# Optimization experiments

Measured on AMD Instinct MI355X. Metric: run time of the kernel, lower is better.

The kernel has to match this reference:

```python
import jax, jax.numpy as jnp
import numpy as np

N_NODES = 100000
N_EDGES = 1600000
IN_DIM = 128
OUT_DIM = 128
N_HEADS = 4


def setup_inputs() -> dict:
    key = jax.random.key(0)
    k1, k2, k3, k4, k5 = jax.random.split(key, 5)
    h = jax.random.normal(k1, (N_NODES, IN_DIM), dtype=jnp.float32)
    src = jax.random.randint(k2, (N_EDGES,), 0, N_NODES, dtype=jnp.int32)
    dst = jax.random.randint(k3, (N_EDGES,), 0, N_NODES, dtype=jnp.int32)
    s = 1.0 / np.sqrt(IN_DIM)
    W_self = jax.random.normal(k4, (N_HEADS, IN_DIM, OUT_DIM), dtype=jnp.float32) * s
    W_neigh = jax.random.normal(k5, (N_HEADS, IN_DIM, OUT_DIM), dtype=jnp.float32) * s
    b = jnp.zeros((N_HEADS, OUT_DIM), dtype=jnp.float32)
    return {"h": h, "src": src, "dst": dst, "W_self": W_self, "W_neigh": W_neigh, "b": b}


def reference(h, src, dst, W_self, W_neigh, b):
    # Mean neighbor aggregation (shared across heads: SAGEConv 'mean' aggregates
    # raw features, then applies per-head linear layers).
    neigh_sum = jax.ops.segment_sum(h[src], dst, num_segments=N_NODES)   # [N, d_in]
    deg = jax.ops.segment_sum(jnp.ones_like(src, dtype=h.dtype), dst,
                              num_segments=N_NODES)                      # [N]
    h_neigh = neigh_sum / jnp.maximum(deg, 1.0)[:, None]                  # [N, d_in]

    # Per-head: fc_self(h_dst) + fc_neigh(h_neigh) + bias -> [H, N, d_out]
    out = (jnp.einsum('nd,hdo->hno', h, W_self)
           + jnp.einsum('nd,hdo->hno', h_neigh, W_neigh)
           + b[:, None, :])
    # merge='mean': average heads
    return jnp.mean(out, axis=0)  # [N, d_out]
```

## Files before the change

kernel.cpp:

```cpp
#include <hip/hip_runtime.h>

#define N_NODES 100000
#define N_EDGES 1600000
#define DIM 128
#define NH 4

#define NPB 512
#define NB 196
#define CAP 12288
#define BCHUNK 8192
#define BEPT 32
#define NBLK ((N_EDGES + BCHUNK - 1) / BCHUNK)

typedef __attribute__((ext_vector_type(8))) short bf16x8;
typedef __attribute__((ext_vector_type(4))) float f32x4;
typedef __attribute__((ext_vector_type(8))) unsigned short u16x8;

#define B_BCUR   0u
#define B_ROWOFF 4096u
#define B_CSR    405504u
#define B_WPACK  6805504u
#define B_BAVG   6871040u
#define B_HB     6871552u
#define NEED_BF16 32869376ull

__device__ inline unsigned short f2bf(float x) {
    union { float f; unsigned u; } v; v.f = x;
    unsigned r = v.u + 0x7fffu + ((v.u >> 16) & 1u);
    return (unsigned short)(r >> 16);
}

template <bool BF>
__global__ __launch_bounds__(256) void prep_kernel(
    const float* __restrict__ h, unsigned short* __restrict__ hb,
    const float* __restrict__ Ws, const float* __restrict__ Wn,
    const float* __restrict__ b, unsigned short* __restrict__ wpack,
    float* __restrict__ bavg, int* __restrict__ bcur) {
    const int t = threadIdx.x;
    if (blockIdx.x == 0) bcur[t] = t * CAP;
    int i = blockIdx.x * 256 + t;
    if (i < DIM * DIM) {
        float s = 0.f, n = 0.f;
#pragma unroll
        for (int hh = 0; hh < NH; ++hh) {
            s += Ws[hh * DIM * DIM + i];
            n += Wn[hh * DIM * DIM + i];
        }
        s *= 0.25f; n *= 0.25f;
        int k = i >> 7, o = i & 127;
        int nt = o >> 4, lanelo = o & 15;
        int ks = k >> 5, lanehi = (k & 31) >> 3, e = k & 7;
        int pos = (((nt * 4 + ks) * 64) + lanehi * 16 + lanelo) * 8 + e;
        wpack[pos] = f2bf(s);
        wpack[16384 + pos] = f2bf(n);
    }
    if (i < DIM) {
        float bb = 0.f;
#pragma unroll
        for (int hh = 0; hh < NH; ++hh) bb += b[hh * DIM + i];
        bavg[i] = 0.25f * bb;
    }
    if (BF) {
        const float4* p = reinterpret_cast<const float4*>(h) + (size_t)i * 2;
        float4 a = p[0], c = p[1];
        u16x8 r;
        r[0] = f2bf(a.x); r[1] = f2bf(a.y); r[2] = f2bf(a.z); r[3] = f2bf(a.w);
        r[4] = f2bf(c.x); r[5] = f2bf(c.y); r[6] = f2bf(c.z); r[7] = f2bf(c.w);
        reinterpret_cast<u16x8*>(hb)[i] = r;
    }
}

__global__ __launch_bounds__(256) void bucket_scatter_kernel(const int* __restrict__ src,
                                                             const int* __restrict__ dst,
                                                             int* __restrict__ bcur,
                                                             int* __restrict__ ebuf) {
    __shared__ int stage[BCHUNK];
    __shared__ unsigned char bkt[BCHUNK];
    __shared__ int lc[256], lbase[256], lpos[256];
    int t = threadIdx.x;
    lc[t] = 0;
    lpos[t] = 0;
    __syncthreads();
    int e0 = blockIdx.x * BCHUNK;
#pragma unroll 4
    for (int j = 0; j < BEPT; ++j) {
        int e = e0 + j * 256 + t;
        if (e < N_EDGES) {
            int d = dst[e];
            stage[j * 256 + t] = (src[e] << 9) | (d & (NPB - 1));
            bkt[j * 256 + t] = (unsigned char)(d >> 9);
            atomicAdd(&lc[d >> 9], 1);
        }
    }
    __syncthreads();
    if (lc[t]) lbase[t] = atomicAdd(&bcur[t], lc[t]);
    __syncthreads();
#pragma unroll 4
    for (int j = 0; j < BEPT; ++j) {
        int e = e0 + j * 256 + t;
        if (e < N_EDGES) {
            int bb = bkt[j * 256 + t];
            int o = atomicAdd(&lpos[bb], 1);
            ebuf[lbase[bb] + o] = stage[j * 256 + t];
        }
    }
}

__global__ __launch_bounds__(256) void csr_build_kernel(const int* __restrict__ bcur,
                                                        const int* __restrict__ ebuf,
                                                        int* __restrict__ rowoff,
                                                        int* __restrict__ csr) {
    __shared__ int hh[NPB], off[NPB], cur[NPB], ss[256];
    int b = blockIdx.x, t = threadIdx.x;
    int cnt = bcur[b] - b * CAP;
    int ibase = b * CAP;
    ss[t] = bcur[t] - t * CAP;
    __syncthreads();
    for (int o = 1; o < 256; o <<= 1) {
        int add = (t >= o) ? ss[t - o] : 0;
        __syncthreads();
        ss[t] += add;
        __syncthreads();
    }
    int obase = ss[b] - cnt;
    hh[t] = 0; hh[t + 256] = 0;
    cur[t] = 0; cur[t + 256] = 0;
    __syncthreads();
    for (int i = t; i < cnt; i += 256) atomicAdd(&hh[ebuf[ibase + i] & (NPB - 1)], 1);
    __syncthreads();
    int e0 = hh[2 * t], e1 = hh[2 * t + 1];
    ss[t] = e0 + e1;
    __syncthreads();
    for (int o = 1; o < 256; o <<= 1) {
        int add = (t >= o) ? ss[t - o] : 0;
        __syncthreads();
        ss[t] += add;
        __syncthreads();
    }
    int ex = ss[t] - (e0 + e1);
    off[2 * t] = ex;
    off[2 * t + 1] = ex + e0;
    __syncthreads();
    int n0 = b * NPB;
#pragma unroll
    for (int k = 0; k < 2; ++k) {
        int s2 = 2 * t + k;
        int n = n0 + s2;
        int dgv = (k == 0) ? e0 : e1;
        if (n < N_NODES) rowoff[n] = ((obase + off[s2]) << 9) | min(dgv, 511);
    }
    for (int i = t; i < cnt; i += 256) {
        int p = ebuf[ibase + i];
        int nl = p & (NPB - 1);
        int o = atomicAdd(&cur[nl], 1);
        csr[obase + off[nl] + o] = p >> 9;
    }
}

template <bool BF>
__global__ __launch_bounds__(1024, 8) void gather_gemm_kernel(
    const float* __restrict__ h, const unsigned short* __restrict__ hb,
    const int* __restrict__ rowoff, const int* __restrict__ csr,
    float* __restrict__ out, const unsigned short* __restrict__ wpack,
    const float* __restrict__ bavg) {
    __shared__ unsigned short hnl[16][DIM + 8];
    const int lane = threadIdx.x & 63;
    const int w = threadIdx.x >> 6;
    const int nb = blockIdx.x * 16;

    {
        const int node = nb + w;
        const int g = lane >> 4;
        const int c = lane & 15;
        const int pw = rowoff[node];
        const int lo = pw >> 9, dg = pw & 511, hi = lo + dg;
        float a0 = 0.f, a1 = 0.f, a2 = 0.f, a3 = 0.f;
        float a4 = 0.f, a5 = 0.f, a6 = 0.f, a7 = 0.f;
        if (BF) {
            int k = lo + g;
            for (; k + 4 < hi; k += 8) {
                int s0 = csr[k], s1 = csr[k + 4];
                uint4 v = *reinterpret_cast<const uint4*>(hb + (size_t)s0 * DIM + c * 8);
                uint4 u = *reinterpret_cast<const uint4*>(hb + (size_t)s1 * DIM + c * 8);
                a0 += __uint_as_float(v.x << 16) + __uint_as_float(u.x << 16);
                a1 += __uint_as_float(v.x & 0xffff0000u) + __uint_as_float(u.x & 0xffff0000u);
                a2 += __uint_as_float(v.y << 16) + __uint_as_float(u.y << 16);
                a3 += __uint_as_float(v.y & 0xffff0000u) + __uint_as_float(u.y & 0xffff0000u);
                a4 += __uint_as_float(v.z << 16) + __uint_as_float(u.z << 16);
                a5 += __uint_as_float(v.z & 0xffff0000u) + __uint_as_float(u.z & 0xffff0000u);
                a6 += __uint_as_float(v.w << 16) + __uint_as_float(u.w << 16);
                a7 += __uint_as_float(v.w & 0xffff0000u) + __uint_as_float(u.w & 0xffff0000u);
            }
            if (k < hi) {
                uint4 v = *reinterpret_cast<const uint4*>(hb + (size_t)csr[k] * DIM + c * 8);
                a0 += __uint_as_float(v.x << 16);
                a1 += __uint_as_float(v.x & 0xffff0000u);
                a2 += __uint_as_float(v.y << 16);
                a3 += __uint_as_float(v.y & 0xffff0000u);
                a4 += __uint_as_float(v.z << 16);
                a5 += __uint_as_float(v.z & 0xffff0000u);
                a6 += __uint_as_float(v.w << 16);
                a7 += __uint_as_float(v.w & 0xffff0000u);
            }
        } else {
            for (int k = lo + g; k < hi; k += 4) {
                const float4* p = reinterpret_cast<const float4*>(h + (size_t)csr[k] * DIM + c * 8);
                float4 x = p[0], y = p[1];
                a0 += x.x; a1 += x.y; a2 += x.z; a3 += x.w;
                a4 += y.x; a5 += y.y; a6 += y.z; a7 += y.w;
            }
        }
        a0 += __shfl_xor(a0, 16, 64); a0 += __shfl_xor(a0, 32, 64);
        a1 += __shfl_xor(a1, 16, 64); a1 += __shfl_xor(a1, 32, 64);
        a2 += __shfl_xor(a2, 16, 64); a2 += __shfl_xor(a2, 32, 64);
        a3 += __shfl_xor(a3, 16, 64); a3 += __shfl_xor(a3, 32, 64);
        a4 += __shfl_xor(a4, 16, 64); a4 += __shfl_xor(a4, 32, 64);
        a5 += __shfl_xor(a5, 16, 64); a5 += __shfl_xor(a5, 32, 64);
        a6 += __shfl_xor(a6, 16, 64); a6 += __shfl_xor(a6, 32, 64);
        a7 += __shfl_xor(a7, 16, 64); a7 += __shfl_xor(a7, 32, 64);
        if (g == 0) {
            float inv = 1.0f / (float)max(dg, 1);
            u16x8 rr;
            rr[0] = f2bf(a0 * inv); rr[1] = f2bf(a1 * inv);
            rr[2] = f2bf(a2 * inv); rr[3] = f2bf(a3 * inv);
            rr[4] = f2bf(a4 * inv); rr[5] = f2bf(a5 * inv);
            rr[6] = f2bf(a6 * inv); rr[7] = f2bf(a7 * inv);
            *reinterpret_cast<u16x8*>(&hnl[w][c * 8]) = rr;
        }
    }
    __syncthreads();

    if (w < 8) {
        const int nt = w;
        const int khi = lane >> 4;
        const int rowc = nb + (lane & 15);
        f32x4 acc = {};
        const unsigned short* wn_p = wpack + 16384;
#pragma unroll
        for (int ks = 0; ks < 4; ++ks) {
            const int k0 = ks * 32 + khi * 8;
            bf16x8 ha;
            if (BF) {
                ha = *reinterpret_cast<const bf16x8*>(hb + (size_t)rowc * DIM + k0);
            } else {
                const float4* hp = reinterpret_cast<const float4*>(h + (size_t)rowc * DIM + k0);
                float4 x = hp[0], y = hp[1];
                ha[0] = (short)f2bf(x.x); ha[1] = (short)f2bf(x.y);
                ha[2] = (short)f2bf(x.z); ha[3] = (short)f2bf(x.w);
                ha[4] = (short)f2bf(y.x); ha[5] = (short)f2bf(y.y);
                ha[6] = (short)f2bf(y.z); ha[7] = (short)f2bf(y.w);
            }
            bf16x8 na = *reinterpret_cast<const bf16x8*>(&hnl[lane & 15][k0]);
            bf16x8 bs = *reinterpret_cast<const bf16x8*>(wpack + (size_t)(((nt * 4 + ks) * 64 + lane) * 8));
            acc = __builtin_amdgcn_mfma_f32_16x16x32_bf16(ha, bs, acc, 0, 0, 0);
            bf16x8 bn = *reinterpret_cast<const bf16x8*>(wn_p + (size_t)(((nt * 4 + ks) * 64 + lane) * 8));
            acc = __builtin_amdgcn_mfma_f32_16x16x32_bf16(na, bn, acc, 0, 0, 0);
        }
        const int o = nt * 16 + (lane & 15);
        const float bb = bavg[o];
        const int r0 = nb + khi * 4;
#pragma unroll
        for (int r = 0; r < 4; ++r)
            out[(size_t)(r0 + r) * DIM + o] = acc[r] + bb;
    }
}

extern "C" void kernel_launch(void* const* d_in, const int* in_sizes, int n_in,
                              void* d_out, int out_size, void* d_ws, size_t ws_size,
                              hipStream_t stream) {
    const float* h  = (const float*)d_in[0];
    const int* src  = (const int*)d_in[1];
    const int* dst  = (const int*)d_in[2];
    const float* Ws = (const float*)d_in[3];
    const float* Wn = (const float*)d_in[4];
    const float* b  = (const float*)d_in[5];
    float* out = (float*)d_out;

    char* ws = (char*)d_ws;
    int* bcur   = (int*)(ws + B_BCUR);
    int* rowoff = (int*)(ws + B_ROWOFF);
    int* csr    = (int*)(ws + B_CSR);
    unsigned short* wpack = (unsigned short*)(ws + B_WPACK);
    float* bavg = (float*)(ws + B_BAVG);
    unsigned short* hb = (unsigned short*)(ws + B_HB);
    int* ebuf   = (int*)d_out;

    const bool bf = (ws_size >= NEED_BF16);

    if (bf)
        prep_kernel<true><<<(N_NODES * DIM / 8) / 256, 256, 0, stream>>>(h, hb, Ws, Wn, b, wpack, bavg, bcur);
    else
        prep_kernel<false><<<64, 256, 0, stream>>>(h, hb, Ws, Wn, b, wpack, bavg, bcur);
    bucket_scatter_kernel<<<NBLK, 256, 0, stream>>>(src, dst, bcur, ebuf);
    csr_build_kernel<<<NB, 256, 0, stream>>>(bcur, ebuf, rowoff, csr);
    const int fused_blocks = N_NODES / 16;
    if (bf)
        gather_gemm_kernel<true><<<fused_blocks, 1024, 0, stream>>>(h, hb, rowoff, csr, out, wpack, bavg);
    else
        gather_gemm_kernel<false><<<fused_blocks, 1024, 0, stream>>>(h, hb, rowoff, csr, out, wpack, bavg);
}
```

Before: 155.9 us.

## Merge prep into scatter, split gather from GEMM with interleaved self-matmul blocks

Folds the weight/bias packing and bf16 conversion of h into the bucket-scatter kernel as extra blocks, replacing the init writes of bcur with a memset. Breaks the fused 1024-thread gather+GEMM into a 256-thread gather kernel, whose grid interleaves blocks that compute the self-projection into bf16 scratch in the output buffer, and a separate final GEMM that adds the neighbour projection and bias. The aim is better occupancy and less idle MFMA work during the gather, and fewer launches for the small prep work. The cost is an extra kernel launch and a round trip through the output buffer for the intermediates.

```diff
diff --git a/kernel.cpp b/kernel.cpp
--- a/kernel.cpp
+++ b/kernel.cpp
@@ -10,7 +10,11 @@
 #define CAP 12288
 #define BCHUNK 8192
 #define BEPT 32
-#define NBLK ((N_EDGES + BCHUNK - 1) / BCHUNK)
+#define NBLK 196
+#define CVT_BLKS 256
+#define GB 25000
+#define SMB 1563
+#define FUSED_GRID (17 * SMB)
 
 typedef __attribute__((ext_vector_type(8))) short bf16x8;
 typedef __attribute__((ext_vector_type(4))) float f32x4;
@@ -31,53 +35,53 @@
 }
 
 template <bool BF>
-__global__ __launch_bounds__(256) void prep_kernel(
+__global__ __launch_bounds__(256) void prep_scatter_kernel(
+    const int* __restrict__ src, const int* __restrict__ dst,
+    int* __restrict__ bcur, int* __restrict__ ebuf,
     const float* __restrict__ h, unsigned short* __restrict__ hb,
     const float* __restrict__ Ws, const float* __restrict__ Wn,
     const float* __restrict__ b, unsigned short* __restrict__ wpack,
-    float* __restrict__ bavg, int* __restrict__ bcur) {
+    float* __restrict__ bavg) {
     const int t = threadIdx.x;
-    if (blockIdx.x == 0) bcur[t] = t * CAP;
-    int i = blockIdx.x * 256 + t;
-    if (i < DIM * DIM) {
-        float s = 0.f, n = 0.f;
-#pragma unroll
-        for (int hh = 0; hh < NH; ++hh) {
-            s += Ws[hh * DIM * DIM + i];
-            n += Wn[hh * DIM * DIM + i];
-        }
-        s *= 0.25f; n *= 0.25f;
-        int k = i >> 7, o = i & 127;
-        int nt = o >> 4, lanelo = o & 15;
-        int ks = k >> 5, lanehi = (k & 31) >> 3, e = k & 7;
-        int pos = (((nt * 4 + ks) * 64) + lanehi * 16 + lanelo) * 8 + e;
-        wpack[pos] = f2bf(s);
-        wpack[16384 + pos] = f2bf(n);
-    }
-    if (i < DIM) {
-        float bb = 0.f;
-#pragma unroll
-        for (int hh = 0; hh < NH; ++hh) bb += b[hh * DIM + i];
-        bavg[i] = 0.25f * bb;
-    }
-    if (BF) {
-        const float4* p = reinterpret_cast<const float4*>(h) + (size_t)i * 2;
-        float4 a = p[0], c = p[1];
-        u16x8 r;
-        r[0] = f2bf(a.x); r[1] = f2bf(a.y); r[2] = f2bf(a.z); r[3] = f2bf(a.w);
-        r[4] = f2bf(c.x); r[5] = f2bf(c.y); r[6] = f2bf(c.z); r[7] = f2bf(c.w);
-        reinterpret_cast<u16x8*>(hb)[i] = r;
-    }
-}
-
-__global__ __launch_bounds__(256) void bucket_scatter_kernel(const int* __restrict__ src,
-                                                             const int* __restrict__ dst,
-                                                             int* __restrict__ bcur,
-                                                             int* __restrict__ ebuf) {
+    if (blockIdx.x >= NBLK) {
+        const int pb = blockIdx.x - NBLK;
+        int i = pb * 256 + t;
+        if (i < DIM * DIM) {
+            float s = 0.f, n = 0.f;
+#pragma unroll
+            for (int hh = 0; hh < NH; ++hh) {
+                s += Ws[hh * DIM * DIM + i];
+                n += Wn[hh * DIM * DIM + i];
+            }
+            s *= 0.25f; n *= 0.25f;
+            int k = i >> 7, o = i & 127;
+            int nt = o >> 4, lanelo = o & 15;
+            int ks = k >> 5, lanehi = (k & 31) >> 3, e = k & 7;
+            int pos = (((nt * 4 + ks) * 64) + lanehi * 16 + lanelo) * 8 + e;
+            wpack[pos] = f2bf(s);
+            wpack[16384 + pos] = f2bf(n);
+        }
+        if (i < DIM) {
+            float bb = 0.f;
+#pragma unroll
+            for (int hh = 0; hh < NH; ++hh) bb += b[hh * DIM + i];
+            bavg[i] = 0.25f * bb;
+        }
+        if (BF) {
+            for (int c8 = i; c8 < N_NODES * DIM / 8; c8 += CVT_BLKS * 256) {
+                const float4* p = reinterpret_cast<const float4*>(h) + (size_t)c8 * 2;
+                float4 a = p[0], c = p[1];
+                u16x8 r;
+                r[0] = f2bf(a.x); r[1] = f2bf(a.y); r[2] = f2bf(a.z); r[3] = f2bf(a.w);
+                r[4] = f2bf(c.x); r[5] = f2bf(c.y); r[6] = f2bf(c.z); r[7] = f2bf(c.w);
+                reinterpret_cast<u16x8*>(hb)[c8] = r;
+            }
+        }
+        return;
+    }
     __shared__ int stage[BCHUNK];
     __shared__ unsigned char bkt[BCHUNK];
     __shared__ int lc[256], lbase[256], lpos[256];
-    int t = threadIdx.x;
     lc[t] = 0;
     lpos[t] = 0;
     __syncthreads();
@@ -93,7 +97,7 @@
         }
     }
     __syncthreads();
-    if (lc[t]) lbase[t] = atomicAdd(&bcur[t], lc[t]);
+    if (lc[t]) lbase[t] = t * CAP + atomicAdd(&bcur[t], lc[t]);
     __syncthreads();
 #pragma unroll 4
     for (int j = 0; j < BEPT; ++j) {
@@ -112,9 +116,9 @@
                                                         int* __restrict__ csr) {
     __shared__ int hh[NPB], off[NPB], cur[NPB], ss[256];
     int b = blockIdx.x, t = threadIdx.x;
-    int cnt = bcur[b] - b * CAP;
+    int cnt = bcur[b];
     int ibase = b * CAP;
-    ss[t] = bcur[t] - t * CAP;
+    ss[t] = bcur[t];
     __syncthreads();
     for (int o = 1; o < 256; o <<= 1) {
         int add = (t >= o) ? ss[t - o] : 0;
@@ -158,110 +162,202 @@
 }
 
 template <bool BF>
-__global__ __launch_bounds__(1024, 8) void gather_gemm_kernel(
+__global__ __launch_bounds__(256) void gather_selfmm_kernel(
     const float* __restrict__ h, const unsigned short* __restrict__ hb,
     const int* __restrict__ rowoff, const int* __restrict__ csr,
-    float* __restrict__ out, const unsigned short* __restrict__ wpack,
-    const float* __restrict__ bavg) {
-    __shared__ unsigned short hnl[16][DIM + 8];
-    const int lane = threadIdx.x & 63;
-    const int w = threadIdx.x >> 6;
-    const int nb = blockIdx.x * 16;
-
-    {
-        const int node = nb + w;
-        const int g = lane >> 4;
-        const int c = lane & 15;
-        const int pw = rowoff[node];
-        const int lo = pw >> 9, dg = pw & 511, hi = lo + dg;
-        float a0 = 0.f, a1 = 0.f, a2 = 0.f, a3 = 0.f;
-        float a4 = 0.f, a5 = 0.f, a6 = 0.f, a7 = 0.f;
+    float* __restrict__ out, const unsigned short* __restrict__ wpack) {
+    const int bid = blockIdx.x;
+    const int t = threadIdx.x;
+    if (bid % 17 == 0) {
+        if (!BF) return;
+        const int sb = bid / 17;
+        const int lane = t & 63;
+        const int wid = t >> 6;
+        const int node_base = sb * 64 + wid * 16;
+        const int rowc = min(node_base + (lane & 15), N_NODES - 1);
+        const int khi = lane >> 4;
+        f32x4 acc[8] = {};
+#pragma unroll
+        for (int ks = 0; ks < 4; ++ks) {
+            const int k0 = ks * 32 + khi * 8;
+            bf16x8 ha = *reinterpret_cast<const bf16x8*>(hb + (size_t)rowc * DIM + k0);
+#pragma unroll
+            for (int nt = 0; nt < 8; ++nt) {
+                bf16x8 bs = *reinterpret_cast<const bf16x8*>(
+                    wpack + (size_t)(((nt * 4 + ks) * 64 + lane) * 8));
+                acc[nt] = __builtin_amdgcn_mfma_f32_16x16x32_bf16(ha, bs, acc[nt], 0, 0, 0);
+            }
+        }
+        const int slotrow = sb * 64 + (t >> 2);
+        if (slotrow < N_NODES) {
+            unsigned short* base = reinterpret_cast<unsigned short*>(out) +
+                                   (size_t)slotrow * 256 + 128 + (t & 3) * 32;
+#pragma unroll
+            for (int q = 0; q < 4; ++q) {
+                u16x8 r;
+#pragma unroll
+                for (int j = 0; j < 8; ++j) {
+                    const int pos = q * 8 + j;
+                    r[j] = f2bf(acc[pos >> 2][pos & 3]);
+                }
+                *reinterpret_cast<u16x8*>(base + q * 8) = r;
+            }
+        }
+        return;
+    }
+    const int gid = bid - bid / 17 - 1;
+    if (gid >= GB) return;
+    const int node = gid * 4 + (t >> 6);
+    const int lane = t & 63;
+    const int g = lane >> 4;
+    const int c = lane & 15;
+    const int pw = rowoff[node];
+    const int lo = pw >> 9, dg = pw & 511, hi = lo + dg;
+    float a0 = 0.f, a1 = 0.f, a2 = 0.f, a3 = 0.f;
+    float a4 = 0.f, a5 = 0.f, a6 = 0.f, a7 = 0.f;
+    if (BF) {
+        int k = lo + g;
+        for (; k + 4 < hi; k += 8) {
+            int s0 = csr[k], s1 = csr[k + 4];
+            uint4 v = *reinterpret_cast<const uint4*>(hb + (size_t)s0 * DIM + c * 8);
+            uint4 u = *reinterpret_cast<const uint4*>(hb + (size_t)s1 * DIM + c * 8);
+            a0 += __uint_as_float(v.x << 16) + __uint_as_float(u.x << 16);
+            a1 += __uint_as_float(v.x & 0xffff0000u) + __uint_as_float(u.x & 0xffff0000u);
+            a2 += __uint_as_float(v.y << 16) + __uint_as_float(u.y << 16);
+            a3 += __uint_as_float(v.y & 0xffff0000u) + __uint_as_float(u.y & 0xffff0000u);
+            a4 += __uint_as_float(v.z << 16) + __uint_as_float(u.z << 16);
+            a5 += __uint_as_float(v.z & 0xffff0000u) + __uint_as_float(u.z & 0xffff0000u);
+            a6 += __uint_as_float(v.w << 16) + __uint_as_float(u.w << 16);
+            a7 += __uint_as_float(v.w & 0xffff0000u) + __uint_as_float(u.w & 0xffff0000u);
+        }
+        if (k < hi) {
+            uint4 v = *reinterpret_cast<const uint4*>(hb + (size_t)csr[k] * DIM + c * 8);
+            a0 += __uint_as_float(v.x << 16);
+            a1 += __uint_as_float(v.x & 0xffff0000u);
+            a2 += __uint_as_float(v.y << 16);
+            a3 += __uint_as_float(v.y & 0xffff0000u);
+            a4 += __uint_as_float(v.z << 16);
+            a5 += __uint_as_float(v.z & 0xffff0000u);
+            a6 += __uint_as_float(v.w << 16);
+            a7 += __uint_as_float(v.w & 0xffff0000u);
+        }
+    } else {
+        for (int k = lo + g; k < hi; k += 4) {
+            const float4* p = reinterpret_cast<const float4*>(h + (size_t)csr[k] * DIM + c * 8);
+            float4 x = p[0], y = p[1];
+            a0 += x.x; a1 += x.y; a2 += x.z; a3 += x.w;
+            a4 += y.x; a5 += y.y; a6 += y.z; a7 += y.w;
+        }
+    }
+    a0 += __shfl_xor(a0, 16, 64); a0 += __shfl_xor(a0, 32, 64);
+    a1 += __shfl_xor(a1, 16, 64); a1 += __shfl_xor(a1, 32, 64);
+    a2 += __shfl_xor(a2, 16, 64); a2 += __shfl_xor(a2, 32, 64);
+    a3 += __shfl_xor(a3, 16, 64); a3 += __shfl_xor(a3, 32, 64);
+    a4 += __shfl_xor(a4, 16, 64); a4 += __shfl_xor(a4, 32, 64);
+    a5 += __shfl_xor(a5, 16, 64); a5 += __shfl_xor(a5, 32, 64);
+    a6 += __shfl_xor(a6, 16, 64); a6 += __shfl_xor(a6, 32, 64);
+    a7 += __shfl_xor(a7, 16, 64); a7 += __shfl_xor(a7, 32, 64);
+    float inv = 1.0f / (float)max(dg, 1);
+    if (g == 0) {
         if (BF) {
-            int k = lo + g;
-            for (; k + 4 < hi; k += 8) {
-                int s0 = csr[k], s1 = csr[k + 4];
-                uint4 v = *reinterpret_cast<const uint4*>(hb + (size_t)s0 * DIM + c * 8);
-                uint4 u = *reinterpret_cast<const uint4*>(hb + (size_t)s1 * DIM + c * 8);
-                a0 += __uint_as_float(v.x << 16) + __uint_as_float(u.x << 16);
-                a1 += __uint_as_float(v.x & 0xffff0000u) + __uint_as_float(u.x & 0xffff0000u);
-                a2 += __uint_as_float(v.y << 16) + __uint_as_float(u.y << 16);
-                a3 += __uint_as_float(v.y & 0xffff0000u) + __uint_as_float(u.y & 0xffff0000u);
-                a4 += __uint_as_float(v.z << 16) + __uint_as_float(u.z << 16);
-                a5 += __uint_as_float(v.z & 0xffff0000u) + __uint_as_float(u.z & 0xffff0000u);
-                a6 += __uint_as_float(v.w << 16) + __uint_as_float(u.w << 16);
-                a7 += __uint_as_float(v.w & 0xffff0000u) + __uint_as_float(u.w & 0xffff0000u);
-            }
-            if (k < hi) {
-                uint4 v = *reinterpret_cast<const uint4*>(hb + (size_t)csr[k] * DIM + c * 8);
-                a0 += __uint_as_float(v.x << 16);
-                a1 += __uint_as_float(v.x & 0xffff0000u);
-                a2 += __uint_as_float(v.y << 16);
-                a3 += __uint_as_float(v.y & 0xffff0000u);
-                a4 += __uint_as_float(v.z << 16);
-                a5 += __uint_as_float(v.z & 0xffff0000u);
-                a6 += __uint_as_float(v.w << 16);
-                a7 += __uint_as_float(v.w & 0xffff0000u);
-            }
-        } else {
-            for (int k = lo + g; k < hi; k += 4) {
-                const float4* p = reinterpret_cast<const float4*>(h + (size_t)csr[k] * DIM + c * 8);
-                float4 x = p[0], y = p[1];
-                a0 += x.x; a1 += x.y; a2 += x.z; a3 += x.w;
-                a4 += y.x; a5 += y.y; a6 += y.z; a7 += y.w;
-            }
-        }
-        a0 += __shfl_xor(a0, 16, 64); a0 += __shfl_xor(a0, 32, 64);
-        a1 += __shfl_xor(a1, 16, 64); a1 += __shfl_xor(a1, 32, 64);
-        a2 += __shfl_xor(a2, 16, 64); a2 += __shfl_xor(a2, 32, 64);
-        a3 += __shfl_xor(a3, 16, 64); a3 += __shfl_xor(a3, 32, 64);
-        a4 += __shfl_xor(a4, 16, 64); a4 += __shfl_xor(a4, 32, 64);
-        a5 += __shfl_xor(a5, 16, 64); a5 += __shfl_xor(a5, 32, 64);
-        a6 += __shfl_xor(a6, 16, 64); a6 += __shfl_xor(a6, 32, 64);
-        a7 += __shfl_xor(a7, 16, 64); a7 += __shfl_xor(a7, 32, 64);
-        if (g == 0) {
-            float inv = 1.0f / (float)max(dg, 1);
             u16x8 rr;
             rr[0] = f2bf(a0 * inv); rr[1] = f2bf(a1 * inv);
             rr[2] = f2bf(a2 * inv); rr[3] = f2bf(a3 * inv);
             rr[4] = f2bf(a4 * inv); rr[5] = f2bf(a5 * inv);
             rr[6] = f2bf(a6 * inv); rr[7] = f2bf(a7 * inv);
-            *reinterpret_cast<u16x8*>(&hnl[w][c * 8]) = rr;
-        }
-    }
-    __syncthreads();
-
-    if (w < 8) {
-        const int nt = w;
-        const int khi = lane >> 4;
-        const int rowc = nb + (lane & 15);
-        f32x4 acc = {};
-        const unsigned short* wn_p = wpack + 16384;
-#pragma unroll
-        for (int ks = 0; ks < 4; ++ks) {
-            const int k0 = ks * 32 + khi * 8;
+            *reinterpret_cast<u16x8*>(reinterpret_cast<unsigned short*>(out) +
+                                      (size_t)node * 256 + c * 8) = rr;
+        } else {
+            float4 r0, r1;
+            r0.x = a0 * inv; r0.y = a1 * inv; r0.z = a2 * inv; r0.w = a3 * inv;
+            r1.x = a4 * inv; r1.y = a5 * inv; r1.z = a6 * inv; r1.w = a7 * inv;
+            float4* q = reinterpret_cast<float4*>(out + (size_t)node * DIM + c * 8);
+            q[0] = r0;
+            q[1] = r1;
+        }
+    }
+}
+
+template <bool BF>
+__global__ __launch_bounds__(256) void final_gemm_kernel(
+    const float* __restrict__ h, float* __restrict__ out,
+    const unsigned short* __restrict__ wpack, const float* __restrict__ bavg) {
+    const int lane = threadIdx.x & 63;
+    const int wid = threadIdx.x >> 6;
+    const int node_base = blockIdx.x * 64 + wid * 16;
+    const int rowc = min(node_base + (lane & 15), N_NODES - 1);
+    const int khi = lane >> 4;
+    const unsigned short* us = reinterpret_cast<const unsigned short*>(out);
+    f32x4 acc[8];
+    if (BF) {
+        const int slotrow = blockIdx.x * 64 + (threadIdx.x >> 2);
+        if (slotrow < N_NODES) {
+            const u16x8* base = reinterpret_cast<const u16x8*>(
+                us + (size_t)slotrow * 256 + 128 + (threadIdx.x & 3) * 32);
+#pragma unroll
+            for (int q = 0; q < 4; ++q) {
+                u16x8 r = base[q];
+#pragma unroll
+                for (int j = 0; j < 8; ++j) {
+                    const int pos = q * 8 + j;
+                    acc[pos >> 2][pos & 3] = __uint_as_float(((unsigned)(unsigned short)r[j]) << 16);
+                }
+            }
+        } else {
+#pragma unroll
+            for (int nt = 0; nt < 8; ++nt) acc[nt] = (f32x4){0.f, 0.f, 0.f, 0.f};
+        }
+    } else {
+#pragma unroll
+        for (int nt = 0; nt < 8; ++nt) acc[nt] = (f32x4){0.f, 0.f, 0.f, 0.f};
+    }
+    const unsigned short* wn_p = wpack + 16384;
+#pragma unroll
+    for (int ks = 0; ks < 4; ++ks) {
+        const int k0 = ks * 32 + khi * 8;
+        bf16x8 na;
+        if (BF) {
+            na = *reinterpret_cast<const bf16x8*>(us + (size_t)rowc * 256 + k0);
+        } else {
+            const float4* np0 = reinterpret_cast<const float4*>(out + (size_t)rowc * DIM + k0);
+            float4 u = np0[0], v = np0[1];
+            na[0] = (short)f2bf(u.x); na[1] = (short)f2bf(u.y);
+            na[2] = (short)f2bf(u.z); na[3] = (short)f2bf(u.w);
+            na[4] = (short)f2bf(v.x); na[5] = (short)f2bf(v.y);
+            na[6] = (short)f2bf(v.z); na[7] = (short)f2bf(v.w);
+        }
+#pragma unroll
+        for (int nt = 0; nt < 8; ++nt) {
+            bf16x8 bn = *reinterpret_cast<const bf16x8*>(
+                wn_p + (size_t)(((nt * 4 + ks) * 64 + lane) * 8));
+            acc[nt] = __builtin_amdgcn_mfma_f32_16x16x32_bf16(na, bn, acc[nt], 0, 0, 0);
+        }
+        if (!BF) {
+            const float4* hp = reinterpret_cast<const float4*>(h + (size_t)rowc * DIM + k0);
+            float4 x = hp[0], y = hp[1];
             bf16x8 ha;
-            if (BF) {
-                ha = *reinterpret_cast<const bf16x8*>(hb + (size_t)rowc * DIM + k0);
-            } else {
-                const float4* hp = reinterpret_cast<const float4*>(h + (size_t)rowc * DIM + k0);
-                float4 x = hp[0], y = hp[1];
-                ha[0] = (short)f2bf(x.x); ha[1] = (short)f2bf(x.y);
-                ha[2] = (short)f2bf(x.z); ha[3] = (short)f2bf(x.w);
-                ha[4] = (short)f2bf(y.x); ha[5] = (short)f2bf(y.y);
-                ha[6] = (short)f2bf(y.z); ha[7] = (short)f2bf(y.w);
-            }
-            bf16x8 na = *reinterpret_cast<const bf16x8*>(&hnl[lane & 15][k0]);
-            bf16x8 bs = *reinterpret_cast<const bf16x8*>(wpack + (size_t)(((nt * 4 + ks) * 64 + lane) * 8));
-            acc = __builtin_amdgcn_mfma_f32_16x16x32_bf16(ha, bs, acc, 0, 0, 0);
-            bf16x8 bn = *reinterpret_cast<const bf16x8*>(wn_p + (size_t)(((nt * 4 + ks) * 64 + lane) * 8));
-            acc = __builtin_amdgcn_mfma_f32_16x16x32_bf16(na, bn, acc, 0, 0, 0);
-        }
-        const int o = nt * 16 + (lane & 15);
-        const float bb = bavg[o];
-        const int r0 = nb + khi * 4;
-#pragma unroll
-        for (int r = 0; r < 4; ++r)
-            out[(size_t)(r0 + r) * DIM + o] = acc[r] + bb;
+            ha[0] = (short)f2bf(x.x); ha[1] = (short)f2bf(x.y);
+            ha[2] = (short)f2bf(x.z); ha[3] = (short)f2bf(x.w);
+            ha[4] = (short)f2bf(y.x); ha[5] = (short)f2bf(y.y);
+            ha[6] = (short)f2bf(y.z); ha[7] = (short)f2bf(y.w);
+#pragma unroll
+            for (int nt = 0; nt < 8; ++nt) {
+                bf16x8 bs = *reinterpret_cast<const bf16x8*>(
+                    wpack + (size_t)(((nt * 4 + ks) * 64 + lane) * 8));
+                acc[nt] = __builtin_amdgcn_mfma_f32_16x16x32_bf16(ha, bs, acc[nt], 0, 0, 0);
+            }
+        }
+    }
+    const int r0 = node_base + khi * 4;
+#pragma unroll
+    for (int nt = 0; nt < 8; ++nt) {
+        int o = nt * 16 + (lane & 15);
+        float bb = bavg[o];
+#pragma unroll
+        for (int r = 0; r < 4; ++r) {
+            int nr = r0 + r;
+            if (nr < N_NODES) out[(size_t)nr * DIM + o] = acc[nt][r] + bb;
+        }
     }
 }
 
@@ -287,15 +383,22 @@
 
     const bool bf = (ws_size >= NEED_BF16);
 
+    hipMemsetAsync(bcur, 0, 256 * sizeof(int), stream);
+
     if (bf)
-        prep_kernel<true><<<(N_NODES * DIM / 8) / 256, 256, 0, stream>>>(h, hb, Ws, Wn, b, wpack, bavg, bcur);
+        prep_scatter_kernel<true><<<NBLK + CVT_BLKS, 256, 0, stream>>>(
+            src, dst, bcur, ebuf, h, hb, Ws, Wn, b, wpack, bavg);
     else
-        prep_kernel<false><<<64, 256, 0, stream>>>(h, hb, Ws, Wn, b, wpack, bavg, bcur);
-    bucket_scatter_kernel<<<NBLK, 256, 0, stream>>>(src, dst, bcur, ebuf);
+        prep_scatter_kernel<false><<<NBLK + CVT_BLKS, 256, 0, stream>>>(
+            src, dst, bcur, ebuf, h, hb, Ws, Wn, b, wpack, bavg);
     csr_build_kernel<<<NB, 256, 0, stream>>>(bcur, ebuf, rowoff, csr);
-    const int fused_blocks = N_NODES / 16;
-    if (bf)
-        gather_gemm_kernel<true><<<fused_blocks, 1024, 0, stream>>>(h, hb, rowoff, csr, out, wpack, bavg);
-    else
-        gather_gemm_kernel<false><<<fused_blocks, 1024, 0, stream>>>(h, hb, rowoff, csr, out, wpack, bavg);
-}
+    if (bf) {
+        gather_selfmm_kernel<true><<<FUSED_GRID, 256, 0, stream>>>(
+            h, hb, rowoff, csr, out, wpack);
+        final_gemm_kernel<true><<<SMB, 256, 0, stream>>>(h, out, wpack, bavg);
+    } else {
+        gather_selfmm_kernel<false><<<FUSED_GRID, 256, 0, stream>>>(
+            h, hb, rowoff, csr, out, wpack);
+        final_gemm_kernel<false><<<SMB, 256, 0, stream>>>(h, out, wpack, bavg);
+    }
+}
```

Result: slower. 178.3 us (+14.4%).
